# Performance work log

Hardware: AMD Instinct MI355X
Metric: run time of the kernel (lower is better)

The kernel has to match this reference:

```python
import jax, jax.numpy as jnp
import numpy as np

B, T, U = 4, 256, 64
D_ENC, D_PRED, HDIM, V = 640, 640, 640, 1024


def setup_inputs() -> dict:
    key = jax.random.key(0)
    ks = jax.random.split(key, 8)
    s_enc = 1.0 / np.sqrt(D_ENC)
    s_pred = 1.0 / np.sqrt(D_PRED)
    s_h = 1.0 / np.sqrt(HDIM)
    return {
        "enc_out": jax.random.normal(ks[0], (B, T, D_ENC), jnp.float32),
        "pred_out": jax.random.normal(ks[1], (B, U, D_PRED), jnp.float32),
        "W_enc": jax.random.uniform(ks[2], (D_ENC, HDIM), jnp.float32, -s_enc, s_enc),
        "b_enc": jax.random.uniform(ks[3], (HDIM,), jnp.float32, -s_enc, s_enc),
        "W_pred": jax.random.uniform(ks[4], (D_PRED, HDIM), jnp.float32, -s_pred, s_pred),
        "b_pred": jax.random.uniform(ks[5], (HDIM,), jnp.float32, -s_pred, s_pred),
        "W_fc": jax.random.uniform(ks[6], (HDIM, V), jnp.float32, -s_h, s_h),
        "b_fc": jax.random.uniform(ks[7], (V,), jnp.float32, -s_h, s_h),
    }


def reference(enc_out, pred_out, W_enc, b_enc, W_pred, b_pred, W_fc, b_fc):
    # project encoder and predictor to joint hidden dim
    enc = jnp.einsum("btd,dh->bth", enc_out, W_enc) + b_enc      # (B,T,H)
    pred = jnp.einsum("bud,dh->buh", pred_out, W_pred) + b_pred  # (B,U,H)
    # broadcast add -> (B,T,U,H), tanh, project to vocab
    joint = jnp.tanh(enc[:, :, None, :] + pred[:, None, :, :])
    logits = jnp.einsum("btuh,hv->btuv", joint, W_fc) + b_fc      # (B,T,U,V)
    return jax.nn.log_softmax(logits, axis=-1)
```

## Files before the change

### kernel.cpp

```cpp
#include <hip/hip_runtime.h>


#define BB 4
#define TT 256
#define UU 64
#define HH 640
#define VV 1024

typedef __attribute__((ext_vector_type(8))) short bf16x8_t;
typedef __attribute__((ext_vector_type(4))) float f32x4_t;

__device__ __forceinline__ unsigned short f2bf(float x) {
    unsigned int u = __float_as_uint(x);
    u += 0x7fffu + ((u >> 16) & 1u);
    return (unsigned short)(u >> 16);
}

__device__ __forceinline__ float tanh_fast(float x) {
    float e = __expf(2.0f * x);
    return 1.0f - 2.0f / (e + 1.0f);
}

__global__ __launch_bounds__(256) void swizzle_wfc(const float* __restrict__ Wfc,
                                                   short* __restrict__ swz) {
    const int idx  = blockIdx.x * 256 + threadIdx.x;
    const int lane = idx & 63;
    const int nt   = (idx >> 6) & 63;
    const int kt   = idx >> 12;
    const int kb   = kt * 32 + (lane >> 4) * 8;
    const int n    = nt * 16 + (lane & 15);
    bf16x8_t v;
#pragma unroll
    for (int j = 0; j < 8; ++j)
        v[j] = (short)f2bf(Wfc[(size_t)(kb + j) * VV + n]);
    *(bf16x8_t*)(swz + (size_t)idx * 8) = v;
}

__global__ __launch_bounds__(256) void proj_gemm(const float* __restrict__ X,
                                                 const float* __restrict__ W,
                                                 const float* __restrict__ bias,
                                                 float* __restrict__ C) {
    __shared__ float As[32][68];
    __shared__ float Bs[32][68];
    const int tid = threadIdx.x;
    const int m0  = blockIdx.x * 64;
    const int h0  = blockIdx.y * 64;
    const int tx  = tid & 15;
    const int ty  = tid >> 4;
    float accr[4][4] = {{0.f, 0.f, 0.f, 0.f}};

    for (int k0 = 0; k0 < HH; k0 += 32) {
        __syncthreads();
#pragma unroll
        for (int p = 0; p < 8; ++p) {
            int idx = p * 256 + tid;
            As[idx & 31][idx >> 5] = X[(size_t)(m0 + (idx >> 5)) * HH + k0 + (idx & 31)];
            Bs[idx >> 6][idx & 63] = W[(size_t)(k0 + (idx >> 6)) * HH + h0 + (idx & 63)];
        }
        __syncthreads();
#pragma unroll
        for (int kk = 0; kk < 32; ++kk) {
            const float4 a  = *(const float4*)&As[kk][ty * 4];
            const float4 bb = *(const float4*)&Bs[kk][tx * 4];
            accr[0][0] += a.x * bb.x; accr[0][1] += a.x * bb.y; accr[0][2] += a.x * bb.z; accr[0][3] += a.x * bb.w;
            accr[1][0] += a.y * bb.x; accr[1][1] += a.y * bb.y; accr[1][2] += a.y * bb.z; accr[1][3] += a.y * bb.w;
            accr[2][0] += a.z * bb.x; accr[2][1] += a.z * bb.y; accr[2][2] += a.z * bb.z; accr[2][3] += a.z * bb.w;
            accr[3][0] += a.w * bb.x; accr[3][1] += a.w * bb.y; accr[3][2] += a.w * bb.z; accr[3][3] += a.w * bb.w;
        }
    }
    const float4 bv = *(const float4*)&bias[h0 + tx * 4];
#pragma unroll
    for (int i = 0; i < 4; ++i) {
        float4 o;
        o.x = accr[i][0] + bv.x;
        o.y = accr[i][1] + bv.y;
        o.z = accr[i][2] + bv.z;
        o.w = accr[i][3] + bv.w;
        *(float4*)&C[(size_t)(m0 + ty * 4 + i) * HH + h0 + tx * 4] = o;
    }
}

#define SJ 328

__global__ __launch_bounds__(512) void joint_kernel(const float* __restrict__ enc,
                                                    const float* __restrict__ pred,
                                                    const short* __restrict__ swzW,
                                                    const float* __restrict__ b_fc,
                                                    float* __restrict__ out) {
    __shared__ unsigned short jtile[64 * SJ];
    __shared__ float stats[8][64][2];
    __shared__ float logZ[64];

    const int bt   = blockIdx.x;
    const int b    = bt >> 8;
    const int tid  = threadIdx.x;
    const int wave = tid >> 6;
    const int lane = tid & 63;
    const int quad = lane >> 4;
    const int l15  = lane & 15;
    const int n0   = wave * 128;

    const float* encrow = enc + (size_t)bt * HH;
    const float* predb  = pred + (size_t)b * UU * HH;

    float bfc[8];
#pragma unroll
    for (int nt = 0; nt < 8; ++nt) bfc[nt] = b_fc[n0 + nt * 16 + l15];

    f32x4_t acc[4][8];
#pragma unroll
    for (int mt = 0; mt < 4; ++mt)
#pragma unroll
        for (int nt = 0; nt < 8; ++nt)
            acc[mt][nt] = (f32x4_t){0.f, 0.f, 0.f, 0.f};

    for (int phase = 0; phase < 2; ++phase) {
        const int kbase = phase * 320;
        __syncthreads();
        for (int i = tid; i < 64 * 80; i += 512) {
            const int u  = i / 80;
            const int k4 = (i - u * 80) * 4;
            const float4 e = *(const float4*)(encrow + kbase + k4);
            const float4 p = *(const float4*)(predb + (size_t)u * HH + kbase + k4);
            ushort4 h;
            h.x = f2bf(tanh_fast(e.x + p.x));
            h.y = f2bf(tanh_fast(e.y + p.y));
            h.z = f2bf(tanh_fast(e.z + p.z));
            h.w = f2bf(tanh_fast(e.w + p.w));
            *(ushort4*)(jtile + u * SJ + k4) = h;
        }
        __syncthreads();

        for (int kc = 0; kc < 10; ++kc) {
            bf16x8_t af[4];
#pragma unroll
            for (int mt = 0; mt < 4; ++mt)
                af[mt] = *(const bf16x8_t*)((const short*)jtile + (mt * 16 + l15) * SJ + kc * 32 + quad * 8);
            const short* bbase = swzW + (size_t)(((phase * 10 + kc) * 64 + wave * 8) * 64 + lane) * 8;
            bf16x8_t bf[8];
#pragma unroll
            for (int nt = 0; nt < 8; ++nt)
                bf[nt] = *(const bf16x8_t*)(bbase + nt * 512);
#pragma unroll
            for (int mt = 0; mt < 4; ++mt)
#pragma unroll
                for (int nt = 0; nt < 8; ++nt)
                    acc[mt][nt] = __builtin_amdgcn_mfma_f32_16x16x32_bf16(af[mt], bf[nt], acc[mt][nt], 0, 0, 0);
        }
    }

#pragma unroll
    for (int mt = 0; mt < 4; ++mt) {
#pragma unroll
        for (int r = 0; r < 4; ++r) {
            float v[8];
            float vmax = -1e30f;
#pragma unroll
            for (int nt = 0; nt < 8; ++nt) {
                v[nt] = acc[mt][nt][r] + bfc[nt];
                vmax  = fmaxf(vmax, v[nt]);
            }
            float s = 0.f;
#pragma unroll
            for (int nt = 0; nt < 8; ++nt) s += __expf(v[nt] - vmax);
#pragma unroll
            for (int off = 1; off < 16; off <<= 1) {
                const float om = __shfl_xor(vmax, off);
                const float os = __shfl_xor(s, off);
                const float nm = fmaxf(vmax, om);
                s    = s * __expf(vmax - nm) + os * __expf(om - nm);
                vmax = nm;
            }
            if (l15 == 0) {
                const int row = mt * 16 + quad * 4 + r;
                stats[wave][row][0] = vmax;
                stats[wave][row][1] = s;
            }
        }
    }
    __syncthreads();
    if (tid < 64) {
        float M = -1e30f;
#pragma unroll
        for (int w = 0; w < 8; ++w) M = fmaxf(M, stats[w][tid][0]);
        float S = 0.f;
#pragma unroll
        for (int w = 0; w < 8; ++w) S += stats[w][tid][1] * __expf(stats[w][tid][0] - M);
        logZ[tid] = M + __logf(S);
    }
    __syncthreads();

    float* orow = out + (size_t)bt * (UU * VV);
#pragma unroll
    for (int mt = 0; mt < 4; ++mt) {
#pragma unroll
        for (int r = 0; r < 4; ++r) {
            const int row = mt * 16 + quad * 4 + r;
            const float lz = logZ[row];
#pragma unroll
            for (int nt = 0; nt < 8; ++nt)
                orow[(size_t)row * VV + n0 + nt * 16 + l15] = acc[mt][nt][r] + bfc[nt] - lz;
        }
    }
}

extern "C" void kernel_launch(void* const* d_in, const int* in_sizes, int n_in,
                              void* d_out, int out_size, void* d_ws, size_t ws_size,
                              hipStream_t stream) {
    const float* enc_out  = (const float*)d_in[0];
    const float* pred_out = (const float*)d_in[1];
    const float* W_enc    = (const float*)d_in[2];
    const float* b_enc    = (const float*)d_in[3];
    const float* W_pred   = (const float*)d_in[4];
    const float* b_pred   = (const float*)d_in[5];
    const float* W_fc     = (const float*)d_in[6];
    const float* b_fc     = (const float*)d_in[7];
    float* out = (float*)d_out;

    char* ws = (char*)d_ws;
    short* swzW = (short*)ws;
    float* encp = (float*)(ws + 1310720);
    float* predp = (float*)(ws + 1310720 + 2621440);

    swizzle_wfc<<<320, 256, 0, stream>>>(W_fc, swzW);
    proj_gemm<<<dim3(16, 10), 256, 0, stream>>>(enc_out, W_enc, b_enc, encp);
    proj_gemm<<<dim3(4, 10), 256, 0, stream>>>(pred_out, W_pred, b_pred, predp);
    joint_kernel<<<1024, 512, 0, stream>>>(encp, predp, swzW, b_fc, out);
}
```

Baseline: 470.7 us.

## Persistent joint blocks, fragment-ordered LDS tile, merged projection launches

The joint kernel now launches 256 blocks, and each block loops over 4 (b,t) rows instead of handling one row per block. The LDS joint tile is stored in MFMA fragment order so each lane reads its A fragment contiguously, and block barriers become lgkmcnt wait plus s_barrier. The two projection GEMMs are merged into one launch, and launch_bounds asks for 2 blocks per CU. The intent is to cut launch and block-scheduling overhead and LDS bank conflicts. The cost is less parallelism per launch (256 blocks for 256 CUs) and possible register pressure limiting occupancy.

```diff
diff --git a/kernel.cpp b/kernel.cpp
--- a/kernel.cpp
+++ b/kernel.cpp
@@ -19,6 +19,10 @@
 __device__ __forceinline__ float tanh_fast(float x) {
     float e = __expf(2.0f * x);
     return 1.0f - 2.0f / (e + 1.0f);
+}
+
+__device__ __forceinline__ void barrier_lds() {
+    asm volatile("s_waitcnt lgkmcnt(0)\n\ts_barrier" ::: "memory");
 }
 
 __global__ __launch_bounds__(256) void swizzle_wfc(const float* __restrict__ Wfc,
@@ -36,14 +40,23 @@
     *(bf16x8_t*)(swz + (size_t)idx * 8) = v;
 }
 
-__global__ __launch_bounds__(256) void proj_gemm(const float* __restrict__ X,
-                                                 const float* __restrict__ W,
-                                                 const float* __restrict__ bias,
-                                                 float* __restrict__ C) {
+__global__ __launch_bounds__(256) void proj_both(const float* __restrict__ enc,
+                                                 const float* __restrict__ pred,
+                                                 const float* __restrict__ Wenc,
+                                                 const float* __restrict__ benc,
+                                                 const float* __restrict__ Wpred,
+                                                 const float* __restrict__ bpred,
+                                                 float* __restrict__ Cenc,
+                                                 float* __restrict__ Cpred) {
     __shared__ float As[32][68];
     __shared__ float Bs[32][68];
+    const int bx = blockIdx.x;
+    const float *X, *W, *bias;
+    float* C;
+    int m0;
+    if (bx < 16) { X = enc;  W = Wenc;  bias = benc;  C = Cenc;  m0 = bx * 64; }
+    else         { X = pred; W = Wpred; bias = bpred; C = Cpred; m0 = (bx - 16) * 64; }
     const int tid = threadIdx.x;
-    const int m0  = blockIdx.x * 64;
     const int h0  = blockIdx.y * 64;
     const int tx  = tid & 15;
     const int ty  = tid >> 4;
@@ -80,19 +93,16 @@
     }
 }
 
-#define SJ 328
-
-__global__ __launch_bounds__(512) void joint_kernel(const float* __restrict__ enc,
-                                                    const float* __restrict__ pred,
-                                                    const short* __restrict__ swzW,
-                                                    const float* __restrict__ b_fc,
-                                                    float* __restrict__ out) {
-    __shared__ unsigned short jtile[64 * SJ];
+__global__ __launch_bounds__(512, 2) void joint_kernel(const float* __restrict__ enc,
+                                                       const float* __restrict__ pred,
+                                                       const short* __restrict__ swzW,
+                                                       const float* __restrict__ b_fc,
+                                                       float* __restrict__ out) {
+    __shared__ unsigned short jtile[4 * 10 * 64 * 8];
     __shared__ float stats[8][64][2];
     __shared__ float logZ[64];
 
-    const int bt   = blockIdx.x;
-    const int b    = bt >> 8;
+    const int blk  = blockIdx.x;
     const int tid  = threadIdx.x;
     const int wave = tid >> 6;
     const int lane = tid & 63;
@@ -100,106 +110,114 @@
     const int l15  = lane & 15;
     const int n0   = wave * 128;
 
-    const float* encrow = enc + (size_t)bt * HH;
-    const float* predb  = pred + (size_t)b * UU * HH;
-
     float bfc[8];
 #pragma unroll
     for (int nt = 0; nt < 8; ++nt) bfc[nt] = b_fc[n0 + nt * 16 + l15];
 
-    f32x4_t acc[4][8];
-#pragma unroll
-    for (int mt = 0; mt < 4; ++mt)
-#pragma unroll
-        for (int nt = 0; nt < 8; ++nt)
-            acc[mt][nt] = (f32x4_t){0.f, 0.f, 0.f, 0.f};
-
-    for (int phase = 0; phase < 2; ++phase) {
-        const int kbase = phase * 320;
-        __syncthreads();
-        for (int i = tid; i < 64 * 80; i += 512) {
-            const int u  = i / 80;
-            const int k4 = (i - u * 80) * 4;
-            const float4 e = *(const float4*)(encrow + kbase + k4);
-            const float4 p = *(const float4*)(predb + (size_t)u * HH + kbase + k4);
-            ushort4 h;
-            h.x = f2bf(tanh_fast(e.x + p.x));
-            h.y = f2bf(tanh_fast(e.y + p.y));
-            h.z = f2bf(tanh_fast(e.z + p.z));
-            h.w = f2bf(tanh_fast(e.w + p.w));
-            *(ushort4*)(jtile + u * SJ + k4) = h;
-        }
-        __syncthreads();
-
-        for (int kc = 0; kc < 10; ++kc) {
-            bf16x8_t af[4];
-#pragma unroll
-            for (int mt = 0; mt < 4; ++mt)
-                af[mt] = *(const bf16x8_t*)((const short*)jtile + (mt * 16 + l15) * SJ + kc * 32 + quad * 8);
-            const short* bbase = swzW + (size_t)(((phase * 10 + kc) * 64 + wave * 8) * 64 + lane) * 8;
-            bf16x8_t bf[8];
+    for (int it = 0; it < 4; ++it) {
+        const int bt = blk * 4 + it;
+        const float* encrow = enc + (size_t)bt * HH;
+        const float* predb  = pred + (size_t)(bt >> 8) * UU * HH;
+
+        f32x4_t acc[4][8];
+#pragma unroll
+        for (int mt = 0; mt < 4; ++mt)
 #pragma unroll
             for (int nt = 0; nt < 8; ++nt)
-                bf[nt] = *(const bf16x8_t*)(bbase + nt * 512);
-#pragma unroll
-            for (int mt = 0; mt < 4; ++mt)
+                acc[mt][nt] = (f32x4_t){0.f, 0.f, 0.f, 0.f};
+
+        for (int phase = 0; phase < 2; ++phase) {
+            const int kbase = phase * 320;
+            barrier_lds();
+            for (int i = tid; i < 64 * 80; i += 512) {
+                const int u  = i / 80;
+                const int k4 = (i - u * 80) * 4;
+                const float4 e = *(const float4*)(encrow + kbase + k4);
+                const float4 p = *(const float4*)(predb + (size_t)u * HH + kbase + k4);
+                ushort4 h;
+                h.x = f2bf(tanh_fast(e.x + p.x));
+                h.y = f2bf(tanh_fast(e.y + p.y));
+                h.z = f2bf(tanh_fast(e.z + p.z));
+                h.w = f2bf(tanh_fast(e.w + p.w));
+                const int mt  = u >> 4;
+                const int ul  = u & 15;
+                const int kc  = k4 >> 5;
+                const int qd  = (k4 >> 3) & 3;
+                const int j   = k4 & 7;
+                *(ushort4*)(jtile + (((mt * 10 + kc) * 64 + qd * 16 + ul) << 3) + j) = h;
+            }
+            barrier_lds();
+
+            for (int kc = 0; kc < 10; ++kc) {
+                bf16x8_t af[4];
+#pragma unroll
+                for (int mt = 0; mt < 4; ++mt)
+                    af[mt] = *(const bf16x8_t*)((const short*)jtile + (((mt * 10 + kc) * 64 + lane) << 3));
+                const short* bbase = swzW + (size_t)((((phase * 10 + kc) * 64 + wave * 8) * 64 + lane) << 3);
+                bf16x8_t bf[8];
 #pragma unroll
                 for (int nt = 0; nt < 8; ++nt)
-                    acc[mt][nt] = __builtin_amdgcn_mfma_f32_16x16x32_bf16(af[mt], bf[nt], acc[mt][nt], 0, 0, 0);
-        }
-    }
-
-#pragma unroll
-    for (int mt = 0; mt < 4; ++mt) {
-#pragma unroll
-        for (int r = 0; r < 4; ++r) {
-            float v[8];
-            float vmax = -1e30f;
-#pragma unroll
-            for (int nt = 0; nt < 8; ++nt) {
-                v[nt] = acc[mt][nt][r] + bfc[nt];
-                vmax  = fmaxf(vmax, v[nt]);
-            }
-            float s = 0.f;
-#pragma unroll
-            for (int nt = 0; nt < 8; ++nt) s += __expf(v[nt] - vmax);
-#pragma unroll
-            for (int off = 1; off < 16; off <<= 1) {
-                const float om = __shfl_xor(vmax, off);
-                const float os = __shfl_xor(s, off);
-                const float nm = fmaxf(vmax, om);
-                s    = s * __expf(vmax - nm) + os * __expf(om - nm);
-                vmax = nm;
-            }
-            if (l15 == 0) {
+                    bf[nt] = *(const bf16x8_t*)(bbase + nt * 512);
+#pragma unroll
+                for (int mt = 0; mt < 4; ++mt)
+#pragma unroll
+                    for (int nt = 0; nt < 8; ++nt)
+                        acc[mt][nt] = __builtin_amdgcn_mfma_f32_16x16x32_bf16(af[mt], bf[nt], acc[mt][nt], 0, 0, 0);
+            }
+        }
+
+#pragma unroll
+        for (int mt = 0; mt < 4; ++mt) {
+#pragma unroll
+            for (int r = 0; r < 4; ++r) {
+                float v[8];
+                float vmax = -1e30f;
+#pragma unroll
+                for (int nt = 0; nt < 8; ++nt) {
+                    v[nt] = acc[mt][nt][r] + bfc[nt];
+                    vmax  = fmaxf(vmax, v[nt]);
+                }
+                float s = 0.f;
+#pragma unroll
+                for (int nt = 0; nt < 8; ++nt) s += __expf(v[nt] - vmax);
+#pragma unroll
+                for (int off = 1; off < 16; off <<= 1) {
+                    const float om = __shfl_xor(vmax, off);
+                    const float os = __shfl_xor(s, off);
+                    const float nm = fmaxf(vmax, om);
+                    s    = s * __expf(vmax - nm) + os * __expf(om - nm);
+                    vmax = nm;
+                }
+                if (l15 == 0) {
+                    const int row = mt * 16 + quad * 4 + r;
+                    stats[wave][row][0] = vmax;
+                    stats[wave][row][1] = s;
+                }
+            }
+        }
+        barrier_lds();
+        if (tid < 64) {
+            float M = -1e30f;
+#pragma unroll
+            for (int w = 0; w < 8; ++w) M = fmaxf(M, stats[w][tid][0]);
+            float S = 0.f;
+#pragma unroll
+            for (int w = 0; w < 8; ++w) S += stats[w][tid][1] * __expf(stats[w][tid][0] - M);
+            logZ[tid] = M + __logf(S);
+        }
+        barrier_lds();
+
+        float* orow = out + (size_t)bt * (UU * VV);
+#pragma unroll
+        for (int mt = 0; mt < 4; ++mt) {
+#pragma unroll
+            for (int r = 0; r < 4; ++r) {
                 const int row = mt * 16 + quad * 4 + r;
-                stats[wave][row][0] = vmax;
-                stats[wave][row][1] = s;
-            }
-        }
-    }
-    __syncthreads();
-    if (tid < 64) {
-        float M = -1e30f;
-#pragma unroll
-        for (int w = 0; w < 8; ++w) M = fmaxf(M, stats[w][tid][0]);
-        float S = 0.f;
-#pragma unroll
-        for (int w = 0; w < 8; ++w) S += stats[w][tid][1] * __expf(stats[w][tid][0] - M);
-        logZ[tid] = M + __logf(S);
-    }
-    __syncthreads();
-
-    float* orow = out + (size_t)bt * (UU * VV);
-#pragma unroll
-    for (int mt = 0; mt < 4; ++mt) {
-#pragma unroll
-        for (int r = 0; r < 4; ++r) {
-            const int row = mt * 16 + quad * 4 + r;
-            const float lz = logZ[row];
-#pragma unroll
-            for (int nt = 0; nt < 8; ++nt)
-                orow[(size_t)row * VV + n0 + nt * 16 + l15] = acc[mt][nt][r] + bfc[nt] - lz;
+                const float lz = logZ[row];
+#pragma unroll
+                for (int nt = 0; nt < 8; ++nt)
+                    orow[(size_t)row * VV + n0 + nt * 16 + l15] = acc[mt][nt][r] + bfc[nt] - lz;
+            }
         }
     }
 }
@@ -218,12 +236,13 @@
     float* out = (float*)d_out;
 
     char* ws = (char*)d_ws;
-    short* swzW = (short*)ws;
-    float* encp = (float*)(ws + 1310720);
+    short* swzW  = (short*)ws;
+    float* encp  = (float*)(ws + 1310720);
     float* predp = (float*)(ws + 1310720 + 2621440);
 
     swizzle_wfc<<<320, 256, 0, stream>>>(W_fc, swzW);
-    proj_gemm<<<dim3(16, 10), 256, 0, stream>>>(enc_out, W_enc, b_enc, encp);
-    proj_gemm<<<dim3(4, 10), 256, 0, stream>>>(pred_out, W_pred, b_pred, predp);
-    joint_kernel<<<1024, 512, 0, stream>>>(encp, predp, swzW, b_fc, out);
-}
+    proj_both<<<dim3(20, 10), 256, 0, stream>>>(enc_out, pred_out,
+                                                W_enc, b_enc, W_pred, b_pred,
+                                                encp, predp);
+    joint_kernel<<<256, 512, 0, stream>>>(encp, predp, swzW, b_fc, out);
+}
```

After: 431.9 us. 1.09x faster.
